# Kernel optimization log

Hardware: AMD Instinct MI355X
Metric: run time of the kernel (lower is better)

Reference implementation:

```python
import jax, jax.numpy as jnp
import numpy as np

N_EMBD = 1024
N_HEAD = 16
HEAD_DIM = N_EMBD // N_HEAD
D_FF = 4 * N_EMBD
B, T = 2, 2048


def setup_inputs() -> dict:
    key = jax.random.key(0)
    ks = jax.random.split(key, 16)
    s = 0.02
    d = {
        'x': jax.random.normal(ks[0], (B, T, N_EMBD), jnp.float32),
        'ln1_g': jnp.ones((N_EMBD,), jnp.float32),
        'ln1_b': jnp.zeros((N_EMBD,), jnp.float32),
        'Wq': jax.random.normal(ks[1], (N_EMBD, N_EMBD), jnp.float32) * s,
        'bq': jnp.zeros((N_EMBD,), jnp.float32),
        'Wk': jax.random.normal(ks[2], (N_EMBD, N_EMBD), jnp.float32) * s,
        'bk': jnp.zeros((N_EMBD,), jnp.float32),
        'Wv': jax.random.normal(ks[3], (N_EMBD, N_EMBD), jnp.float32) * s,
        'bv': jnp.zeros((N_EMBD,), jnp.float32),
        'Wo': jax.random.normal(ks[4], (N_EMBD, N_EMBD), jnp.float32) * s,
        'bo': jnp.zeros((N_EMBD,), jnp.float32),
        'ln2_g': jnp.ones((N_EMBD,), jnp.float32),
        'ln2_b': jnp.zeros((N_EMBD,), jnp.float32),
        'W1': jax.random.normal(ks[5], (N_EMBD, D_FF), jnp.float32) * s,
        'b1': jnp.zeros((D_FF,), jnp.float32),
        'W2': jax.random.normal(ks[6], (D_FF, N_EMBD), jnp.float32) * s,
        'b2': jnp.zeros((N_EMBD,), jnp.float32),
    }
    return d


def _layernorm(x, g, b, eps=1e-5):
    mu = jnp.mean(x, axis=-1, keepdims=True)
    var = jnp.var(x, axis=-1, keepdims=True)
    return (x - mu) * jax.lax.rsqrt(var + eps) * g + b


def _attention(x, Wq, bq, Wk, bk, Wv, bv, Wo, bo):
    b, t, c = x.shape
    q = (x @ Wq + bq).reshape(b, t, N_HEAD, HEAD_DIM).transpose(0, 2, 1, 3)
    k = (x @ Wk + bk).reshape(b, t, N_HEAD, HEAD_DIM).transpose(0, 2, 1, 3)
    v = (x @ Wv + bv).reshape(b, t, N_HEAD, HEAD_DIM).transpose(0, 2, 1, 3)
    att = jnp.einsum('bhqd,bhkd->bhqk', q, k) / jnp.sqrt(jnp.float32(HEAD_DIM))
    causal = jnp.tril(jnp.ones((t, t), bool))
    att = jnp.where(causal[None, None], att, -jnp.inf)
    att = jax.nn.softmax(att, axis=-1)
    y = jnp.einsum('bhqk,bhkd->bhqd', att, v)
    y = y.transpose(0, 2, 1, 3).reshape(b, t, c)
    return y @ Wo + bo


def reference(x, ln1_g, ln1_b, Wq, bq, Wk, bk, Wv, bv, Wo, bo, ln2_g, ln2_b, W1, b1, W2, b2):
    x = x + _attention(_layernorm(x, ln1_g, ln1_b), Wq, bq, Wk, bk, Wv, bv, Wo, bo)
    h = _layernorm(x, ln2_g, ln2_b)
    h = jax.nn.gelu(h @ W1 + b1, approximate=False) @ W2 + b2
    return x + h
```

## Files before the change

kernel.cpp:

```cpp
#include <hip/hip_runtime.h>
#include <hip/hip_bf16.h>

typedef __hip_bfloat16 bf16;
using bf16x8 = __attribute__((ext_vector_type(8))) short;
using f32x4  = __attribute__((ext_vector_type(4))) float;
using f32x16 = __attribute__((ext_vector_type(16))) float;

#define TSEQ 2048
#define NH   16
#define HD   64
#define NC   1024
#define DFF  4096
#define NROWS 4096

__device__ __forceinline__ void load_lds16(const bf16* g, bf16* l) {
  __builtin_amdgcn_global_load_lds(
      (const __attribute__((address_space(1))) unsigned int*)g,
      (__attribute__((address_space(3))) unsigned int*)l, 16, 0, 0);
}

__device__ __forceinline__ float b2f(short s) {
  unsigned int u = ((unsigned int)(unsigned short)s) << 16;
  return __builtin_bit_cast(float, u);
}

__device__ __forceinline__ float gelu_f(float x) {
  float u = 0.7978845608028654f * fmaf(0.044715f * x, x * x, x);
  float e = __expf(2.0f * u);
  float t = 1.0f - 2.0f / (e + 1.0f);
  return 0.5f * x * (1.0f + t);
}

__global__ __launch_bounds__(256)
void ln_cast_kernel(const float* __restrict__ x, const float* __restrict__ g,
                    const float* __restrict__ b, bf16* __restrict__ out) {
  int row = blockIdx.x, tid = threadIdx.x;
  const float4 v = ((const float4*)(x + (size_t)row * NC))[tid];
  float s  = v.x + v.y + v.z + v.w;
  float s2 = v.x*v.x + v.y*v.y + v.z*v.z + v.w*v.w;
#pragma unroll
  for (int m = 1; m < 64; m <<= 1) { s += __shfl_xor(s, m); s2 += __shfl_xor(s2, m); }
  __shared__ float rs[4], rs2[4];
  if ((tid & 63) == 0) { rs[tid >> 6] = s; rs2[tid >> 6] = s2; }
  __syncthreads();
  s  = rs[0] + rs[1] + rs[2] + rs[3];
  s2 = rs2[0] + rs2[1] + rs2[2] + rs2[3];
  float mu   = s * (1.0f / NC);
  float var  = s2 * (1.0f / NC) - mu * mu;
  float rstd = rsqrtf(var + 1e-5f);
  const float4 gv = ((const float4*)g)[tid];
  const float4 bv = ((const float4*)b)[tid];
  bf16* o = out + (size_t)row * NC + tid * 4;
  o[0] = __float2bfloat16((v.x - mu) * rstd * gv.x + bv.x);
  o[1] = __float2bfloat16((v.y - mu) * rstd * gv.y + bv.y);
  o[2] = __float2bfloat16((v.z - mu) * rstd * gv.z + bv.z);
  o[3] = __float2bfloat16((v.w - mu) * rstd * gv.w + bv.w);
}

__global__ __launch_bounds__(256)
void wo_ln_kernel(const float* __restrict__ x, const float* __restrict__ bo,
                  const bf16* __restrict__ P, const float* __restrict__ g,
                  const float* __restrict__ bln, float* __restrict__ x2,
                  bf16* __restrict__ xn2) {
  int row = blockIdx.x, tid = threadIdx.x;
  size_t base = (size_t)row * NC + tid * 4;
  const float4 xv = *(const float4*)(x + base);
  const float4 bv = ((const float4*)bo)[tid];
  short4 p0 = *(const short4*)((const short*)P + base);
  short4 p1 = *(const short4*)((const short*)P + (size_t)NROWS * NC + base);
  float v0 = xv.x + bv.x + b2f(p0.x) + b2f(p1.x);
  float v1 = xv.y + bv.y + b2f(p0.y) + b2f(p1.y);
  float v2 = xv.z + bv.z + b2f(p0.z) + b2f(p1.z);
  float v3 = xv.w + bv.w + b2f(p0.w) + b2f(p1.w);
  float4 ov = {v0, v1, v2, v3};
  *(float4*)(x2 + base) = ov;
  float s  = v0 + v1 + v2 + v3;
  float s2 = v0*v0 + v1*v1 + v2*v2 + v3*v3;
#pragma unroll
  for (int m = 1; m < 64; m <<= 1) { s += __shfl_xor(s, m); s2 += __shfl_xor(s2, m); }
  __shared__ float rs[4], rs2[4];
  if ((tid & 63) == 0) { rs[tid >> 6] = s; rs2[tid >> 6] = s2; }
  __syncthreads();
  s  = rs[0] + rs[1] + rs[2] + rs[3];
  s2 = rs2[0] + rs2[1] + rs2[2] + rs2[3];
  float mu   = s * (1.0f / NC);
  float var  = s2 * (1.0f / NC) - mu * mu;
  float rstd = rsqrtf(var + 1e-5f);
  const float4 gv = ((const float4*)g)[tid];
  const float4 lv = ((const float4*)bln)[tid];
  bf16* o = xn2 + base;
  o[0] = __float2bfloat16((v0 - mu) * rstd * gv.x + lv.x);
  o[1] = __float2bfloat16((v1 - mu) * rstd * gv.y + lv.y);
  o[2] = __float2bfloat16((v2 - mu) * rstd * gv.z + lv.z);
  o[3] = __float2bfloat16((v3 - mu) * rstd * gv.w + lv.w);
}

__global__ __launch_bounds__(256)
void w2_final_kernel(const float* __restrict__ x2, const float* __restrict__ b2,
                     const bf16* __restrict__ P, float* __restrict__ out) {
  int row = blockIdx.x, tid = threadIdx.x;
  size_t base = (size_t)row * NC + tid * 4;
  const float4 xv = *(const float4*)(x2 + base);
  const float4 bv = ((const float4*)b2)[tid];
  float a0 = xv.x + bv.x, a1 = xv.y + bv.y, a2 = xv.z + bv.z, a3 = xv.w + bv.w;
#pragma unroll
  for (int z = 0; z < 4; ++z) {
    short4 p = *(const short4*)((const short*)P + (size_t)z * NROWS * NC + base);
    a0 += b2f(p.x); a1 += b2f(p.y); a2 += b2f(p.z); a3 += b2f(p.w);
  }
  float4 ov = {a0, a1, a2, a3};
  *(float4*)(out + base) = ov;
}

__global__ __launch_bounds__(256)
void transpose_all_kernel(const float* __restrict__ Wq, const float* __restrict__ Wk,
                          const float* __restrict__ Wv, const float* __restrict__ Wo,
                          const float* __restrict__ W1, const float* __restrict__ W2,
                          bf16* __restrict__ WqkvoT, bf16* __restrict__ W1T,
                          bf16* __restrict__ W2T) {
  int bid = blockIdx.x;
  const float* W; bf16* Wt; int K, N, nx, tile;
  if (bid < 4096) {
    int z = bid >> 10; tile = bid & 1023;
    W = (z == 0) ? Wq : (z == 1) ? Wk : (z == 2) ? Wv : Wo;
    Wt = WqkvoT + (size_t)z * NC * NC; K = NC; N = NC; nx = 32;
  } else if (bid < 8192) {
    tile = bid - 4096; W = W1; Wt = W1T; K = NC; N = DFF; nx = 128;
  } else {
    tile = bid - 8192; W = W2; Wt = W2T; K = DFF; N = NC; nx = 32;
  }
  int n0 = (tile % nx) * 32, k0 = (tile / nx) * 32;
  __shared__ float t[32][33];
  int tx = threadIdx.x, ty = threadIdx.y;
#pragma unroll
  for (int i = 0; i < 4; ++i)
    t[ty + i * 8][tx] = W[(size_t)(k0 + ty + i * 8) * N + n0 + tx];
  __syncthreads();
#pragma unroll
  for (int i = 0; i < 4; ++i)
    Wt[(size_t)(n0 + ty + i * 8) * K + k0 + tx] = __float2bfloat16(t[tx][ty + i * 8]);
}

#define MODE_GELU 4
#define MODE_QKV  5
#define MODE_PART 6

template <int MODE>
__global__ __launch_bounds__(256)
void gemm_bt(const bf16* __restrict__ A, const bf16* __restrict__ Bt,
             const float* __restrict__ bias, const float* __restrict__ bias2,
             const float* __restrict__ bias3,
             void* __restrict__ outp, void* __restrict__ out2, void* __restrict__ out3,
             int M, int N, int K, int KS) {
  __shared__ bf16 As[128 * 64];
  __shared__ bf16 Bs[128 * 64];
  int tid  = threadIdx.x;
  int w    = tid >> 6;
  int lane = tid & 63;
  int l32  = lane & 31;
  int khalf = lane >> 5;
  int sx   = lane & 7;
  int waveM = (w >> 1) * 64, waveN = (w & 1) * 64;

  int gN = gridDim.x, gM = gridDim.y;
  int pid = blockIdx.y * gN + blockIdx.x;
  int npg = 8 * gN;
  int gid = pid / npg;
  int fm  = gid * 8;
  int gsz = min(gM - fm, 8);
  int bm = (fm + (pid % gsz)) * 128;
  int bn = ((pid % npg) / gsz) * 128;

  int k_beg = blockIdx.z * KS;

  const bf16* pA[4]; const bf16* pB[4];
#pragma unroll
  for (int i = 0; i < 4; ++i) {
    int p = i * 256 + tid;
    int row = p >> 3;
    int lc = (p & 7) ^ (row & 7);
    pA[i] = A  + (size_t)(bm + row) * K + k_beg + lc * 8;
    pB[i] = Bt + (size_t)(bn + row) * K + k_beg + lc * 8;
  }

  f32x16 acc[2][2];
#pragma unroll
  for (int mi = 0; mi < 2; ++mi)
#pragma unroll
    for (int ni = 0; ni < 2; ++ni)
#pragma unroll
      for (int r = 0; r < 16; ++r) acc[mi][ni][r] = 0.f;

  for (int kt = 0; kt < KS; kt += 64) {
    __syncthreads();
#pragma unroll
    for (int i = 0; i < 4; ++i) {
      load_lds16(pA[i], &As[(i * 256 + w * 64) * 8]);
      load_lds16(pB[i], &Bs[(i * 256 + w * 64) * 8]);
      pA[i] += 64; pB[i] += 64;
    }
    __syncthreads();
#pragma unroll
    for (int s = 0; s < 4; ++s) {
      int ch = ((s * 2 + khalf) ^ sx) * 8;
      bf16x8 af[2], bfr[2];
#pragma unroll
      for (int mi = 0; mi < 2; ++mi)
        af[mi] = *(const bf16x8*)&As[(waveM + mi * 32 + l32) * 64 + ch];
#pragma unroll
      for (int ni = 0; ni < 2; ++ni)
        bfr[ni] = *(const bf16x8*)&Bs[(waveN + ni * 32 + l32) * 64 + ch];
#pragma unroll
      for (int mi = 0; mi < 2; ++mi)
#pragma unroll
        for (int ni = 0; ni < 2; ++ni)
          acc[mi][ni] = __builtin_amdgcn_mfma_f32_32x32x16_bf16(af[mi], bfr[ni], acc[mi][ni], 0, 0, 0);
    }
  }

  if (MODE == MODE_PART) {
    bf16* dst = (bf16*)outp + (size_t)blockIdx.z * M * N;
#pragma unroll
    for (int mi = 0; mi < 2; ++mi)
#pragma unroll
      for (int ni = 0; ni < 2; ++ni) {
        int col = bn + waveN + ni * 32 + l32;
#pragma unroll
        for (int reg = 0; reg < 16; ++reg) {
          int row = bm + waveM + mi * 32 + (reg & 3) + 8 * (reg >> 2) + 4 * khalf;
          dst[(size_t)row * N + col] = __float2bfloat16(acc[mi][ni][reg]);
        }
      }
  } else if (MODE == MODE_GELU) {
    float bcol[2];
#pragma unroll
    for (int ni = 0; ni < 2; ++ni) bcol[ni] = bias[bn + waveN + ni * 32 + l32];
#pragma unroll
    for (int mi = 0; mi < 2; ++mi)
#pragma unroll
      for (int ni = 0; ni < 2; ++ni) {
        int col = bn + waveN + ni * 32 + l32;
#pragma unroll
        for (int reg = 0; reg < 16; ++reg) {
          int row = bm + waveM + mi * 32 + (reg & 3) + 8 * (reg >> 2) + 4 * khalf;
          ((bf16*)outp)[(size_t)row * N + col] =
              __float2bfloat16(gelu_f(acc[mi][ni][reg] + bcol[ni]));
        }
      }
  } else {
    int seg = bn >> 10;
    int c1b = (bn & (NC - 1)) + waveN;
    const float* bp = (seg == 0) ? bias : (seg == 1) ? bias2 : bias3;
    float bcol[2]; int hh[2], dd[2];
#pragma unroll
    for (int ni = 0; ni < 2; ++ni) {
      int c1 = c1b + ni * 32 + l32;
      bcol[ni] = bp[c1]; hh[ni] = c1 >> 6; dd[ni] = c1 & (HD - 1);
    }
    if (seg < 2) {
      bf16* dst = (seg == 0) ? (bf16*)outp : (bf16*)out2;
#pragma unroll
      for (int mi = 0; mi < 2; ++mi)
#pragma unroll
        for (int reg = 0; reg < 16; ++reg) {
          int row = bm + waveM + mi * 32 + (reg & 3) + 8 * (reg >> 2) + 4 * khalf;
          int bbi = row >> 11, t = row & (TSEQ - 1);
#pragma unroll
          for (int ni = 0; ni < 2; ++ni)
            dst[((size_t)(bbi * NH + hh[ni]) * TSEQ + t) * HD + dd[ni]] =
                __float2bfloat16(acc[mi][ni][reg] + bcol[ni]);
        }
    } else {
      bf16* dst = (bf16*)out3;
#pragma unroll
      for (int mi = 0; mi < 2; ++mi)
#pragma unroll
        for (int reg = 0; reg < 16; ++reg) {
          int row = bm + waveM + mi * 32 + (reg & 3) + 8 * (reg >> 2) + 4 * khalf;
          int bbi = row >> 11, t = row & (TSEQ - 1);
#pragma unroll
          for (int ni = 0; ni < 2; ++ni)
            dst[((size_t)(bbi * NH + hh[ni]) * HD + dd[ni]) * TSEQ + t] =
                __float2bfloat16(acc[mi][ni][reg] + bcol[ni]);
        }
    }
  }
}

__global__ __launch_bounds__(256)
void attn_kernel(const bf16* __restrict__ q, const bf16* __restrict__ k,
                 const bf16* __restrict__ vT, bf16* __restrict__ out) {
  int j = blockIdx.x, h = blockIdx.y, b = blockIdx.z;
  int tid = threadIdx.x, w = tid >> 6, lane = tid & 63;
  int l16 = lane & 15, quad = lane >> 4;
  int tlo = j, thi = 31 - j;
  int qlo0 = tlo * 64 + w * 16;
  int qhi0 = thi * 64 + w * 16;
  const bf16* qp = q  + (size_t)(b * NH + h) * TSEQ * HD;
  const bf16* kp = k  + (size_t)(b * NH + h) * TSEQ * HD;
  const bf16* vp = vT + (size_t)(b * NH + h) * HD * TSEQ;

  __shared__ bf16 Ks[2][64 * 64];
  __shared__ bf16 Vs[2][64 * 64];
  __shared__ bf16 Pw[4][16 * 64];

  bf16x8 qfl[2], qfh[2];
  qfl[0] = *(const bf16x8*)(qp + (size_t)(qlo0 + l16) * HD + quad * 8);
  qfl[1] = *(const bf16x8*)(qp + (size_t)(qlo0 + l16) * HD + 32 + quad * 8);
  qfh[0] = *(const bf16x8*)(qp + (size_t)(qhi0 + l16) * HD + quad * 8);
  qfh[1] = *(const bf16x8*)(qp + (size_t)(qhi0 + l16) * HD + 32 + quad * 8);

  f32x4 ol[4], oh[4];
  float ll[4], lh[4];
#pragma unroll
  for (int i = 0; i < 4; ++i) {
    ol[i] = (f32x4){0.f, 0.f, 0.f, 0.f};
    oh[i] = (f32x4){0.f, 0.f, 0.f, 0.f};
    ll[i] = 0.f; lh[i] = 0.f;
  }

  int lrow = lane >> 3;
  int lc   = (lane & 7) ^ lrow;

  auto stage = [&](int kt, int bi) {
    int kj0 = kt * 64;
#pragma unroll
    for (int i = 0; i < 2; ++i) {
      int c2 = i * 4 + w;
      int row = c2 * 8 + lrow;
      load_lds16(kp + (size_t)(kj0 + row) * HD + lc * 8, &Ks[bi][c2 * 512]);
      load_lds16(vp + (size_t)row * TSEQ + kj0 + lc * 8, &Vs[bi][c2 * 512]);
    }
  };

  auto compute = [&](const bf16x8* qf, int qi0, f32x4* o, float* lacc, int bi, int kj0) {
    float p[4][4];
#pragma unroll
    for (int qq = 0; qq < 4; ++qq) {
      if (kj0 + qq * 16 <= qi0 + 15) {
        f32x4 t = (f32x4){0.f, 0.f, 0.f, 0.f};
        int krow = qq * 16 + l16;
        bf16x8 kf0 = *(const bf16x8*)&Ks[bi][krow * 64 + ((quad       ^ (l16 & 7)) * 8)];
        bf16x8 kf1 = *(const bf16x8*)&Ks[bi][krow * 64 + (((quad + 4) ^ (l16 & 7)) * 8)];
        t = __builtin_amdgcn_mfma_f32_16x16x32_bf16(qf[0], kf0, t, 0, 0, 0);
        t = __builtin_amdgcn_mfma_f32_16x16x32_bf16(qf[1], kf1, t, 0, 0, 0);
        int kj = kj0 + qq * 16 + l16;
#pragma unroll
        for (int r = 0; r < 4; ++r) {
          int qi = qi0 + quad * 4 + r;
          float s = (kj <= qi) ? fmaf(t[r], 0.125f, -8.0f) : -INFINITY;
          p[qq][r] = __expf(s);
          lacc[r] += p[qq][r];
        }
      } else {
#pragma unroll
        for (int r = 0; r < 4; ++r) p[qq][r] = 0.f;
      }
    }
#pragma unroll
    for (int qq = 0; qq < 4; ++qq)
#pragma unroll
      for (int r = 0; r < 4; ++r) {
        int prow = quad * 4 + r;
        int c = qq * 2 + (l16 >> 3);
        Pw[w][prow * 64 + ((c ^ (prow & 7)) * 8) + (l16 & 7)] = __float2bfloat16(p[qq][r]);
      }
#pragma unroll
    for (int tc = 0; tc < 2; ++tc) {
      if (kj0 + tc * 32 <= qi0 + 15) {
        bf16x8 pf = *(const bf16x8*)&Pw[w][l16 * 64 + (((tc * 4 + quad) ^ (l16 & 7)) * 8)];
#pragma unroll
        for (int dn = 0; dn < 4; ++dn) {
          int vrow = dn * 16 + l16;
          bf16x8 vf = *(const bf16x8*)&Vs[bi][vrow * 64 + (((tc * 4 + quad) ^ (l16 & 7)) * 8)];
          o[dn] = __builtin_amdgcn_mfma_f32_16x16x32_bf16(pf, vf, o[dn], 0, 0, 0);
        }
      }
    }
  };

  int nkt = thi + 1;
  stage(0, 0);
  for (int kt = 0; kt < nkt; ++kt) {
    int bi = kt & 1;
    __syncthreads();
    if (kt + 1 < nkt) stage(kt + 1, 1 - bi);
    compute(qfh, qhi0, oh, lh, bi, kt * 64);
    if (kt <= tlo) compute(qfl, qlo0, ol, ll, bi, kt * 64);
  }

#pragma unroll
  for (int m = 1; m < 16; m <<= 1)
#pragma unroll
    for (int r = 0; r < 4; ++r) {
      ll[r] += __shfl_xor(ll[r], m);
      lh[r] += __shfl_xor(lh[r], m);
    }
#pragma unroll
  for (int dn = 0; dn < 4; ++dn)
#pragma unroll
    for (int r = 0; r < 4; ++r) {
      int tl = qlo0 + quad * 4 + r;
      int th = qhi0 + quad * 4 + r;
      out[((size_t)(b * TSEQ + tl)) * NC + h * HD + dn * 16 + l16] = __float2bfloat16(ol[dn][r] / ll[r]);
      out[((size_t)(b * TSEQ + th)) * NC + h * HD + dn * 16 + l16] = __float2bfloat16(oh[dn][r] / lh[r]);
    }
}

extern "C" void kernel_launch(void* const* d_in, const int* in_sizes, int n_in,
                              void* d_out, int out_size, void* d_ws, size_t ws_size,
                              hipStream_t stream) {
  const float* x     = (const float*)d_in[0];
  const float* ln1_g = (const float*)d_in[1];
  const float* ln1_b = (const float*)d_in[2];
  const float* Wq    = (const float*)d_in[3];
  const float* bq    = (const float*)d_in[4];
  const float* Wk    = (const float*)d_in[5];
  const float* bk    = (const float*)d_in[6];
  const float* Wv    = (const float*)d_in[7];
  const float* bv    = (const float*)d_in[8];
  const float* Wo    = (const float*)d_in[9];
  const float* bo    = (const float*)d_in[10];
  const float* ln2_g = (const float*)d_in[11];
  const float* ln2_b = (const float*)d_in[12];
  const float* W1    = (const float*)d_in[13];
  const float* b1    = (const float*)d_in[14];
  const float* W2    = (const float*)d_in[15];
  const float* b2    = (const float*)d_in[16];

  char* ws = (char*)d_ws;
  const size_t MB = 1u << 20;
  bf16* WqkvT = (bf16*)(ws + 0 * MB);
  bf16* W1T  = (bf16*)(ws + 8 * MB);
  bf16* W2T  = (bf16*)(ws + 16 * MB);
  bf16* xn1  = (bf16*)(ws + 24 * MB);
  bf16* qb   = (bf16*)(ws + 32 * MB);
  bf16* kb   = (bf16*)(ws + 40 * MB);
  bf16* vTb  = (bf16*)(ws + 48 * MB);
  bf16* att  = (bf16*)(ws + 56 * MB);
  float* x2  = (float*)(ws + 64 * MB);
  bf16* xn2  = (bf16*)(ws + 80 * MB);
  bf16* h1   = (bf16*)(ws + 88 * MB);
  bf16* woP  = (bf16*)(ws + 88 * MB);
  bf16* w2P  = (bf16*)(ws + 32 * MB);
  bf16* WoT  = WqkvT + 3 * (size_t)NC * NC;

  transpose_all_kernel<<<12288, dim3(32, 8), 0, stream>>>(
      Wq, Wk, Wv, Wo, W1, W2, WqkvT, W1T, W2T);

  ln_cast_kernel<<<NROWS, 256, 0, stream>>>(x, ln1_g, ln1_b, xn1);

  gemm_bt<MODE_QKV><<<dim3(24, 32, 1), 256, 0, stream>>>(
      xn1, WqkvT, bq, bk, bv, qb, kb, vTb, NROWS, 3 * NC, NC, NC);

  attn_kernel<<<dim3(16, NH, 2), 256, 0, stream>>>(qb, kb, vTb, att);

  gemm_bt<MODE_PART><<<dim3(8, 32, 2), 256, 0, stream>>>(
      att, WoT, nullptr, nullptr, nullptr, woP, nullptr, nullptr, NROWS, NC, NC, NC / 2);

  wo_ln_kernel<<<NROWS, 256, 0, stream>>>(x, bo, woP, ln2_g, ln2_b, x2, xn2);

  gemm_bt<MODE_GELU><<<dim3(32, 32, 1), 256, 0, stream>>>(
      xn2, W1T, b1, nullptr, nullptr, h1, nullptr, nullptr, NROWS, DFF, NC, NC);

  gemm_bt<MODE_PART><<<dim3(8, 32, 4), 256, 0, stream>>>(
      h1, W2T, nullptr, nullptr, nullptr, w2P, nullptr, nullptr, NROWS, NC, DFF, DFF / 4);

  w2_final_kernel<<<NROWS, 256, 0, stream>>>(x2, b2, w2P, (float*)d_out);
}
```

Baseline: 366.5 us.

## Fold softmax scale into Q and give each attention block one query tile

The QKV GEMM epilogue now multiplies Q by 1/sqrt(d)*log2(e), so attention can use exp2f directly instead of an fma followed by __expf. The attention kernel no longer pairs a low and a high query tile per block. Each block now handles a single 64-row query tile, the grid doubles, and block order is reversed so the longest causal rows are scheduled first. Off-diagonal key tiles skip the causal mask compare. The fixed -8 offset before the exponential is also dropped, which removes a safeguard against overflow when scores are large. Load balance now depends on the hardware scheduler rather than explicit tile pairing.

```diff
diff --git a/kernel.cpp b/kernel.cpp
--- a/kernel.cpp
+++ b/kernel.cpp
@@ -12,6 +12,8 @@
 #define NC   1024
 #define DFF  4096
 #define NROWS 4096
+
+#define QSCALE 0.18033688011112042f
 
 __device__ __forceinline__ void load_lds16(const bf16* g, bf16* l) {
   __builtin_amdgcn_global_load_lds(
@@ -251,6 +253,7 @@
     int seg = bn >> 10;
     int c1b = (bn & (NC - 1)) + waveN;
     const float* bp = (seg == 0) ? bias : (seg == 1) ? bias2 : bias3;
+    float qs = (seg == 0) ? QSCALE : 1.0f;
     float bcol[2]; int hh[2], dd[2];
 #pragma unroll
     for (int ni = 0; ni < 2; ++ni) {
@@ -268,7 +271,7 @@
 #pragma unroll
           for (int ni = 0; ni < 2; ++ni)
             dst[((size_t)(bbi * NH + hh[ni]) * TSEQ + t) * HD + dd[ni]] =
-                __float2bfloat16(acc[mi][ni][reg] + bcol[ni]);
+                __float2bfloat16((acc[mi][ni][reg] + bcol[ni]) * qs);
         }
     } else {
       bf16* dst = (bf16*)out3;
@@ -290,12 +293,11 @@
 __global__ __launch_bounds__(256)
 void attn_kernel(const bf16* __restrict__ q, const bf16* __restrict__ k,
                  const bf16* __restrict__ vT, bf16* __restrict__ out) {
-  int j = blockIdx.x, h = blockIdx.y, b = blockIdx.z;
+  int J = (int)gridDim.x - 1 - blockIdx.x;
+  int h = blockIdx.y, b = blockIdx.z;
   int tid = threadIdx.x, w = tid >> 6, lane = tid & 63;
   int l16 = lane & 15, quad = lane >> 4;
-  int tlo = j, thi = 31 - j;
-  int qlo0 = tlo * 64 + w * 16;
-  int qhi0 = thi * 64 + w * 16;
+  int qi0 = J * 64 + w * 16;
   const bf16* qp = q  + (size_t)(b * NH + h) * TSEQ * HD;
   const bf16* kp = k  + (size_t)(b * NH + h) * TSEQ * HD;
   const bf16* vp = vT + (size_t)(b * NH + h) * HD * TSEQ;
@@ -304,20 +306,14 @@
   __shared__ bf16 Vs[2][64 * 64];
   __shared__ bf16 Pw[4][16 * 64];
 
-  bf16x8 qfl[2], qfh[2];
-  qfl[0] = *(const bf16x8*)(qp + (size_t)(qlo0 + l16) * HD + quad * 8);
-  qfl[1] = *(const bf16x8*)(qp + (size_t)(qlo0 + l16) * HD + 32 + quad * 8);
-  qfh[0] = *(const bf16x8*)(qp + (size_t)(qhi0 + l16) * HD + quad * 8);
-  qfh[1] = *(const bf16x8*)(qp + (size_t)(qhi0 + l16) * HD + 32 + quad * 8);
-
-  f32x4 ol[4], oh[4];
-  float ll[4], lh[4];
-#pragma unroll
-  for (int i = 0; i < 4; ++i) {
-    ol[i] = (f32x4){0.f, 0.f, 0.f, 0.f};
-    oh[i] = (f32x4){0.f, 0.f, 0.f, 0.f};
-    ll[i] = 0.f; lh[i] = 0.f;
-  }
+  bf16x8 qf[2];
+  qf[0] = *(const bf16x8*)(qp + (size_t)(qi0 + l16) * HD + quad * 8);
+  qf[1] = *(const bf16x8*)(qp + (size_t)(qi0 + l16) * HD + 32 + quad * 8);
+
+  f32x4 o[4];
+  float lacc[4];
+#pragma unroll
+  for (int i = 0; i < 4; ++i) { o[i] = (f32x4){0.f, 0.f, 0.f, 0.f}; lacc[i] = 0.f; }
 
   int lrow = lane >> 3;
   int lc   = (lane & 7) ^ lrow;
@@ -333,24 +329,35 @@
     }
   };
 
-  auto compute = [&](const bf16x8* qf, int qi0, f32x4* o, float* lacc, int bi, int kj0) {
+  for (int kt = 0; kt <= J; ++kt) {
+    int bi = kt & 1;
+    if (kt == 0) stage(0, 0);
+    __syncthreads();
+    if (kt < J) stage(kt + 1, 1 - bi);
+    int kj0 = kt * 64;
+    bool full = (kt < J);
     float p[4][4];
 #pragma unroll
     for (int qq = 0; qq < 4; ++qq) {
-      if (kj0 + qq * 16 <= qi0 + 15) {
+      if (full || kj0 + qq * 16 <= qi0 + 15) {
         f32x4 t = (f32x4){0.f, 0.f, 0.f, 0.f};
         int krow = qq * 16 + l16;
         bf16x8 kf0 = *(const bf16x8*)&Ks[bi][krow * 64 + ((quad       ^ (l16 & 7)) * 8)];
         bf16x8 kf1 = *(const bf16x8*)&Ks[bi][krow * 64 + (((quad + 4) ^ (l16 & 7)) * 8)];
         t = __builtin_amdgcn_mfma_f32_16x16x32_bf16(qf[0], kf0, t, 0, 0, 0);
         t = __builtin_amdgcn_mfma_f32_16x16x32_bf16(qf[1], kf1, t, 0, 0, 0);
-        int kj = kj0 + qq * 16 + l16;
-#pragma unroll
-        for (int r = 0; r < 4; ++r) {
-          int qi = qi0 + quad * 4 + r;
-          float s = (kj <= qi) ? fmaf(t[r], 0.125f, -8.0f) : -INFINITY;
-          p[qq][r] = __expf(s);
-          lacc[r] += p[qq][r];
+        if (full) {
+#pragma unroll
+          for (int r = 0; r < 4; ++r) { p[qq][r] = exp2f(t[r]); lacc[r] += p[qq][r]; }
+        } else {
+          int kj = kj0 + qq * 16 + l16;
+#pragma unroll
+          for (int r = 0; r < 4; ++r) {
+            int qi = qi0 + quad * 4 + r;
+            float s = (kj <= qi) ? t[r] : -INFINITY;
+            p[qq][r] = exp2f(s);
+            lacc[r] += p[qq][r];
+          }
         }
       } else {
 #pragma unroll
@@ -367,7 +374,7 @@
       }
 #pragma unroll
     for (int tc = 0; tc < 2; ++tc) {
-      if (kj0 + tc * 32 <= qi0 + 15) {
+      if (full || kj0 + tc * 32 <= qi0 + 15) {
         bf16x8 pf = *(const bf16x8*)&Pw[w][l16 * 64 + (((tc * 4 + quad) ^ (l16 & 7)) * 8)];
 #pragma unroll
         for (int dn = 0; dn < 4; ++dn) {
@@ -377,33 +384,19 @@
         }
       }
     }
-  };
-
-  int nkt = thi + 1;
-  stage(0, 0);
-  for (int kt = 0; kt < nkt; ++kt) {
-    int bi = kt & 1;
-    __syncthreads();
-    if (kt + 1 < nkt) stage(kt + 1, 1 - bi);
-    compute(qfh, qhi0, oh, lh, bi, kt * 64);
-    if (kt <= tlo) compute(qfl, qlo0, ol, ll, bi, kt * 64);
   }
 
 #pragma unroll
   for (int m = 1; m < 16; m <<= 1)
 #pragma unroll
+    for (int r = 0; r < 4; ++r) lacc[r] += __shfl_xor(lacc[r], m);
+#pragma unroll
+  for (int dn = 0; dn < 4; ++dn)
+#pragma unroll
     for (int r = 0; r < 4; ++r) {
-      ll[r] += __shfl_xor(ll[r], m);
-      lh[r] += __shfl_xor(lh[r], m);
-    }
-#pragma unroll
-  for (int dn = 0; dn < 4; ++dn)
-#pragma unroll
-    for (int r = 0; r < 4; ++r) {
-      int tl = qlo0 + quad * 4 + r;
-      int th = qhi0 + quad * 4 + r;
-      out[((size_t)(b * TSEQ + tl)) * NC + h * HD + dn * 16 + l16] = __float2bfloat16(ol[dn][r] / ll[r]);
-      out[((size_t)(b * TSEQ + th)) * NC + h * HD + dn * 16 + l16] = __float2bfloat16(oh[dn][r] / lh[r]);
+      int t = qi0 + quad * 4 + r;
+      out[((size_t)(b * TSEQ + t)) * NC + h * HD + dn * 16 + l16] =
+          __float2bfloat16(o[dn][r] / lacc[r]);
     }
 }
 
@@ -453,7 +446,7 @@
   gemm_bt<MODE_QKV><<<dim3(24, 32, 1), 256, 0, stream>>>(
       xn1, WqkvT, bq, bk, bv, qb, kb, vTb, NROWS, 3 * NC, NC, NC);
 
-  attn_kernel<<<dim3(16, NH, 2), 256, 0, stream>>>(qb, kb, vTb, att);
+  attn_kernel<<<dim3(32, NH, 2), 256, 0, stream>>>(qb, kb, vTb, att);
 
   gemm_bt<MODE_PART><<<dim3(8, 32, 2), 256, 0, stream>>>(
       att, WoT, nullptr, nullptr, nullptr, woP, nullptr, nullptr, NROWS, NC, NC, NC / 2);
```

Result: slower. 391.8 us (+6.9%).

## Split attention KV range across two blocks with merge kernel, fold scale into Q

Applied to the files above, without the earlier changes.

Doubles the attention grid by assigning even and odd KV tiles to separate blocks, which write unnormalized bf16 partial outputs and row sums; a new merge kernel adds the two partials and normalizes. The softmax scale and log2e are folded into Q at the QKV GEMM epilogue so the inner loop uses exp2f. Fully unmasked tiles also skip the causal-mask comparison. The aim is more parallelism for the 512-block attention launch on a many-CU GPU. In exchange it adds an extra kernel, extra global traffic for the partials, and bf16 rounding of the unnormalized partials.

```diff
diff --git a/kernel.cpp b/kernel.cpp
--- a/kernel.cpp
+++ b/kernel.cpp
@@ -12,6 +12,8 @@
 #define NC   1024
 #define DFF  4096
 #define NROWS 4096
+
+#define QSCALE 0.18033688011112042f
 
 __device__ __forceinline__ void load_lds16(const bf16* g, bf16* l) {
   __builtin_amdgcn_global_load_lds(
@@ -55,6 +57,25 @@
   o[1] = __float2bfloat16((v.y - mu) * rstd * gv.y + bv.y);
   o[2] = __float2bfloat16((v.z - mu) * rstd * gv.z + bv.z);
   o[3] = __float2bfloat16((v.w - mu) * rstd * gv.w + bv.w);
+}
+
+__global__ __launch_bounds__(256)
+void attn_merge_kernel(const bf16* __restrict__ O, const float* __restrict__ L,
+                       bf16* __restrict__ att) {
+  int row = blockIdx.x, tid = threadIdx.x;
+  int b = row >> 11, t = row & (TSEQ - 1);
+  int h = tid >> 4;
+  float l0 = L[((size_t)(0 + b) * NH + h) * TSEQ + t];
+  float l1 = L[((size_t)(2 + b) * NH + h) * TSEQ + t];
+  float rl = 1.0f / (l0 + l1);
+  size_t base = (size_t)row * NC + tid * 4;
+  short4 o0 = *(const short4*)((const short*)O + base);
+  short4 o1 = *(const short4*)((const short*)O + (size_t)NROWS * NC + base);
+  bf16* d = att + base;
+  d[0] = __float2bfloat16((b2f(o0.x) + b2f(o1.x)) * rl);
+  d[1] = __float2bfloat16((b2f(o0.y) + b2f(o1.y)) * rl);
+  d[2] = __float2bfloat16((b2f(o0.z) + b2f(o1.z)) * rl);
+  d[3] = __float2bfloat16((b2f(o0.w) + b2f(o1.w)) * rl);
 }
 
 __global__ __launch_bounds__(256)
@@ -251,6 +272,7 @@
     int seg = bn >> 10;
     int c1b = (bn & (NC - 1)) + waveN;
     const float* bp = (seg == 0) ? bias : (seg == 1) ? bias2 : bias3;
+    float qs = (seg == 0) ? QSCALE : 1.0f;
     float bcol[2]; int hh[2], dd[2];
 #pragma unroll
     for (int ni = 0; ni < 2; ++ni) {
@@ -268,7 +290,7 @@
 #pragma unroll
           for (int ni = 0; ni < 2; ++ni)
             dst[((size_t)(bbi * NH + hh[ni]) * TSEQ + t) * HD + dd[ni]] =
-                __float2bfloat16(acc[mi][ni][reg] + bcol[ni]);
+                __float2bfloat16((acc[mi][ni][reg] + bcol[ni]) * qs);
         }
     } else {
       bf16* dst = (bf16*)out3;
@@ -289,8 +311,10 @@
 
 __global__ __launch_bounds__(256)
 void attn_kernel(const bf16* __restrict__ q, const bf16* __restrict__ k,
-                 const bf16* __restrict__ vT, bf16* __restrict__ out) {
-  int j = blockIdx.x, h = blockIdx.y, b = blockIdx.z;
+                 const bf16* __restrict__ vT, bf16* __restrict__ Opart,
+                 float* __restrict__ Lpart) {
+  int j = blockIdx.x, h = blockIdx.y;
+  int b = blockIdx.z & 1, z = blockIdx.z >> 1;
   int tid = threadIdx.x, w = tid >> 6, lane = tid & 63;
   int l16 = lane & 15, quad = lane >> 4;
   int tlo = j, thi = 31 - j;
@@ -333,24 +357,30 @@
     }
   };
 
-  auto compute = [&](const bf16x8* qf, int qi0, f32x4* o, float* lacc, int bi, int kj0) {
+  auto compute = [&](const bf16x8* qf, int qi0, f32x4* o, float* lacc, int bi, int kj0,
+                     bool full) {
     float p[4][4];
 #pragma unroll
     for (int qq = 0; qq < 4; ++qq) {
-      if (kj0 + qq * 16 <= qi0 + 15) {
+      if (full || kj0 + qq * 16 <= qi0 + 15) {
         f32x4 t = (f32x4){0.f, 0.f, 0.f, 0.f};
         int krow = qq * 16 + l16;
         bf16x8 kf0 = *(const bf16x8*)&Ks[bi][krow * 64 + ((quad       ^ (l16 & 7)) * 8)];
         bf16x8 kf1 = *(const bf16x8*)&Ks[bi][krow * 64 + (((quad + 4) ^ (l16 & 7)) * 8)];
         t = __builtin_amdgcn_mfma_f32_16x16x32_bf16(qf[0], kf0, t, 0, 0, 0);
         t = __builtin_amdgcn_mfma_f32_16x16x32_bf16(qf[1], kf1, t, 0, 0, 0);
-        int kj = kj0 + qq * 16 + l16;
-#pragma unroll
-        for (int r = 0; r < 4; ++r) {
-          int qi = qi0 + quad * 4 + r;
-          float s = (kj <= qi) ? fmaf(t[r], 0.125f, -8.0f) : -INFINITY;
-          p[qq][r] = __expf(s);
-          lacc[r] += p[qq][r];
+        if (full) {
+#pragma unroll
+          for (int r = 0; r < 4; ++r) { p[qq][r] = exp2f(t[r]); lacc[r] += p[qq][r]; }
+        } else {
+          int kj = kj0 + qq * 16 + l16;
+#pragma unroll
+          for (int r = 0; r < 4; ++r) {
+            int qi = qi0 + quad * 4 + r;
+            float s = (kj <= qi) ? t[r] : -INFINITY;
+            p[qq][r] = exp2f(s);
+            lacc[r] += p[qq][r];
+          }
         }
       } else {
 #pragma unroll
@@ -367,7 +397,7 @@
       }
 #pragma unroll
     for (int tc = 0; tc < 2; ++tc) {
-      if (kj0 + tc * 32 <= qi0 + 15) {
+      if (full || kj0 + tc * 32 <= qi0 + 15) {
         bf16x8 pf = *(const bf16x8*)&Pw[w][l16 * 64 + (((tc * 4 + quad) ^ (l16 & 7)) * 8)];
 #pragma unroll
         for (int dn = 0; dn < 4; ++dn) {
@@ -379,14 +409,16 @@
     }
   };
 
-  int nkt = thi + 1;
-  stage(0, 0);
-  for (int kt = 0; kt < nkt; ++kt) {
-    int bi = kt & 1;
+  int nit = (thi - z) / 2 + 1;
+  stage(z, 0);
+  for (int it = 0; it < nit; ++it) {
+    int kt = z + it * 2;
+    int bi = it & 1;
     __syncthreads();
-    if (kt + 1 < nkt) stage(kt + 1, 1 - bi);
-    compute(qfh, qhi0, oh, lh, bi, kt * 64);
-    if (kt <= tlo) compute(qfl, qlo0, ol, ll, bi, kt * 64);
+    if (it + 1 < nit) stage(kt + 2, 1 - bi);
+    int kj0 = kt * 64;
+    compute(qfh, qhi0, oh, lh, bi, kj0, kt < thi);
+    if (kt <= tlo) compute(qfl, qlo0, ol, ll, bi, kj0, kt < tlo);
   }
 
 #pragma unroll
@@ -396,14 +428,22 @@
       ll[r] += __shfl_xor(ll[r], m);
       lh[r] += __shfl_xor(lh[r], m);
     }
+  float* Lp = Lpart + ((size_t)(z * 2 + b) * NH + h) * TSEQ;
+  if (l16 == 0)
+#pragma unroll
+    for (int r = 0; r < 4; ++r) {
+      Lp[qlo0 + quad * 4 + r] = ll[r];
+      Lp[qhi0 + quad * 4 + r] = lh[r];
+    }
+  bf16* Op = Opart + (size_t)z * NROWS * NC;
 #pragma unroll
   for (int dn = 0; dn < 4; ++dn)
 #pragma unroll
     for (int r = 0; r < 4; ++r) {
       int tl = qlo0 + quad * 4 + r;
       int th = qhi0 + quad * 4 + r;
-      out[((size_t)(b * TSEQ + tl)) * NC + h * HD + dn * 16 + l16] = __float2bfloat16(ol[dn][r] / ll[r]);
-      out[((size_t)(b * TSEQ + th)) * NC + h * HD + dn * 16 + l16] = __float2bfloat16(oh[dn][r] / lh[r]);
+      Op[((size_t)(b * TSEQ + tl)) * NC + h * HD + dn * 16 + l16] = __float2bfloat16(ol[dn][r]);
+      Op[((size_t)(b * TSEQ + th)) * NC + h * HD + dn * 16 + l16] = __float2bfloat16(oh[dn][r]);
     }
 }
 
@@ -444,6 +484,8 @@
   bf16* woP  = (bf16*)(ws + 88 * MB);
   bf16* w2P  = (bf16*)(ws + 32 * MB);
   bf16* WoT  = WqkvT + 3 * (size_t)NC * NC;
+  bf16*  attO = (bf16*)(ws + 64 * MB);
+  float* attL = (float*)(ws + 80 * MB);
 
   transpose_all_kernel<<<12288, dim3(32, 8), 0, stream>>>(
       Wq, Wk, Wv, Wo, W1, W2, WqkvT, W1T, W2T);
@@ -453,7 +495,8 @@
   gemm_bt<MODE_QKV><<<dim3(24, 32, 1), 256, 0, stream>>>(
       xn1, WqkvT, bq, bk, bv, qb, kb, vTb, NROWS, 3 * NC, NC, NC);
 
-  attn_kernel<<<dim3(16, NH, 2), 256, 0, stream>>>(qb, kb, vTb, att);
+  attn_kernel<<<dim3(16, NH, 4), 256, 0, stream>>>(qb, kb, vTb, attO, attL);
+  attn_merge_kernel<<<NROWS, 256, 0, stream>>>(attO, attL, att);
 
   gemm_bt<MODE_PART><<<dim3(8, 32, 2), 256, 0, stream>>>(
       att, WoT, nullptr, nullptr, nullptr, woP, nullptr, nullptr, NROWS, NC, NC, NC / 2);
```

New measurement: 371.7 us. About the same (+1.4%).
